# Optimization experiments

Hardware: AMD Instinct MI355X
Metric: run time of the kernel (lower is better)

Reference implementation:

```python
import math
import jax, jax.numpy as jnp
import numpy as np

B, T, D, H, KVH = 2, 2048, 2048, 16, 4
DK = D // H  # 128


def setup_inputs() -> dict:
    key = jax.random.key(0)
    ks = jax.random.split(key, 7)
    q = jax.random.normal(ks[0], (B, T, D), dtype=jnp.float32)
    k = jax.random.normal(ks[1], (B, T, D), dtype=jnp.float32)
    v = jax.random.normal(ks[2], (B, T, D), dtype=jnp.float32)
    # torch Linear weights: (out_features, in_features)
    Wq = jax.random.normal(ks[3], (D, D), dtype=jnp.float32) * 0.02
    Wk = jax.random.normal(ks[4], (KVH * DK, D), dtype=jnp.float32) * 0.02
    Wv = jax.random.normal(ks[5], (KVH * DK, D), dtype=jnp.float32) * 0.02
    Wo = jax.random.normal(ks[6], (D, D), dtype=jnp.float32) * 0.02
    # qk_norm gain, init = log(max_seq_len)
    g = jnp.full((1, H, 1, 1), math.log(2048.0), dtype=jnp.float32)
    return {"q": q, "k": k, "v": v, "Wq": Wq, "Wk": Wk, "Wv": Wv, "Wo": Wo, "g": g}


def _l2norm(x, eps=1e-12):
    # matches torch F.normalize(dim=-1): x / max(||x||, eps)
    n = jnp.sqrt(jnp.sum(x * x, axis=-1, keepdims=True))
    return x / jnp.maximum(n, eps)


def reference(q, k, v, Wq, Wk, Wv, Wo, g):
    b, tq, d = q.shape
    tk = k.shape[1]
    h = g.shape[1]
    dk = d // h
    kvh = Wk.shape[0] // dk

    Q = jnp.einsum('btd,ed->bte', q, Wq).reshape(b, tq, h, dk).transpose(0, 2, 1, 3)     # (B,H,Tq,dk)
    K = jnp.einsum('btd,ed->bte', k, Wk).reshape(b, tk, kvh, dk).transpose(0, 2, 1, 3)   # (B,KVH,Tk,dk)
    V = jnp.einsum('btd,ed->bte', v, Wv).reshape(b, tk, kvh, dk).transpose(0, 2, 1, 3)

    # QK-norm + learned per-head gain
    Q = g * _l2norm(Q)
    K = _l2norm(K)

    # GQA: repeat-interleave kv heads to match query heads (torch enable_gqa)
    rep = h // kvh
    Kr = jnp.repeat(K, rep, axis=1)
    Vr = jnp.repeat(V, rep, axis=1)

    scale = 1.0 / math.sqrt(dk)
    scores = jnp.einsum('bhqd,bhkd->bhqk', Q, Kr) * scale  # (B,H,Tq,Tk)
    causal = jnp.tril(jnp.ones((tq, tk), dtype=bool))
    scores = jnp.where(causal, scores, jnp.finfo(scores.dtype).min)
    A = jax.nn.softmax(scores, axis=-1)
    Y = jnp.einsum('bhqk,bhkd->bhqd', A, Vr)               # (B,H,Tq,dk)
    Y = Y.transpose(0, 2, 1, 3).reshape(b, tq, d)
    return jnp.einsum('btd,ed->bte', Y, Wo)
```

## Files before the change

### kernel.cpp

```cpp
#include <hip/hip_runtime.h>
#include <hip/hip_bf16.h>
#include <stdint.h>

#define B_ 2
#define T_ 2048
#define D_ 2048
#define H_ 16
#define KVH_ 4
#define DK_ 128

typedef __bf16 bf16x8 __attribute__((ext_vector_type(8)));
typedef float f32x4 __attribute__((ext_vector_type(4)));
typedef unsigned short u16x8 __attribute__((ext_vector_type(8)));

typedef __attribute__((address_space(1))) void* gas1_t;
typedef __attribute__((address_space(3))) void* gas3_t;

__device__ __forceinline__ uint16_t f2bf(float f) {
  uint32_t u = __builtin_bit_cast(uint32_t, f);
  u += 0x7FFFu + ((u >> 16) & 1u);
  return (uint16_t)(u >> 16);
}

__device__ __forceinline__ void async16(const void* g, void* l) {
  __builtin_amdgcn_global_load_lds((gas1_t)(uintptr_t)g, (gas3_t)l, 16, 0, 0);
}

__global__ __launch_bounds__(256) void k_cvt_all(const float* __restrict__ q,
                                                 const float* __restrict__ k,
                                                 const float* __restrict__ v,
                                                 const float* __restrict__ wq,
                                                 const float* __restrict__ wk,
                                                 const float* __restrict__ wv,
                                                 const float* __restrict__ wo,
                                                 uint16_t* __restrict__ qb,
                                                 uint16_t* __restrict__ kb,
                                                 uint16_t* __restrict__ vb,
                                                 uint16_t* __restrict__ wqb,
                                                 uint16_t* __restrict__ wkb,
                                                 uint16_t* __restrict__ wvb,
                                                 uint16_t* __restrict__ wob) {
  int gb = blockIdx.x;
  const float* s; uint16_t* d; int base;
  if (gb < 4096)        { s = q;  d = qb;  base = 0; }
  else if (gb < 8192)   { s = k;  d = kb;  base = 4096; }
  else if (gb < 12288)  { s = v;  d = vb;  base = 8192; }
  else if (gb < 14336)  { s = wq; d = wqb; base = 12288; }
  else if (gb < 14848)  { s = wk; d = wkb; base = 14336; }
  else if (gb < 15360)  { s = wv; d = wvb; base = 14848; }
  else                  { s = wo; d = wob; base = 15360; }
  int i = (gb - base) * 256 + threadIdx.x;
  const float4* s4 = (const float4*)s;
  float4 a = s4[(size_t)i * 2], b = s4[(size_t)i * 2 + 1];
  union { uint16_t u[8]; uint4 v; } o;
  o.u[0] = f2bf(a.x); o.u[1] = f2bf(a.y); o.u[2] = f2bf(a.z); o.u[3] = f2bf(a.w);
  o.u[4] = f2bf(b.x); o.u[5] = f2bf(b.y); o.u[6] = f2bf(b.z); o.u[7] = f2bf(b.w);
  ((uint4*)d)[i] = o.v;
}


__global__ __launch_bounds__(256) void k_gemm_bt(const uint16_t* __restrict__ A,
                                                 const uint16_t* __restrict__ Bm,
                                                 float* __restrict__ C,
                                                 int M, int N, int K) {
  __shared__ uint16_t As[2 * 128 * 64];
  __shared__ uint16_t Bs[2 * 128 * 64];
  const int tid = threadIdx.x;
  const int nt = N >> 7;
  const int m0 = (blockIdx.x / nt) << 7;
  const int n0 = (blockIdx.x % nt) << 7;
  const int w = tid >> 6, lane = tid & 63;
  const int wr = (w >> 1) << 6, wc = (w & 1) << 6;
  const int lr = lane & 15;
  const int g16 = ((lane >> 4) << 4);
  const int csw = ((lane & 1) << 6) | (((lane >> 1) & 1) << 5);
  f32x4 acc[4][4] = {};
  const int soff = tid * 16;
  const int scol = ((tid & 7) ^ (((tid >> 3) & 1) << 2) ^ (((tid >> 4) & 1) << 1)) << 3;
  const int srow = tid >> 3;
  const int nk = K >> 6;

  auto stage = [&](int t, int buf) {
    char* Ab = (char*)As + (buf << 14);
    char* Bb = (char*)Bs + (buf << 14);
#pragma unroll
    for (int i = 0; i < 4; ++i) {
      int row = i * 32 + srow;
      async16(A + (size_t)(m0 + row) * K + t * 64 + scol, Ab + i * 4096 + soff);
      async16(Bm + (size_t)(n0 + row) * K + t * 64 + scol, Bb + i * 4096 + soff);
    }
  };

  stage(0, 0);
  asm volatile("s_waitcnt vmcnt(0)" ::: "memory");
  __builtin_amdgcn_s_barrier();
  for (int t = 0; t < nk; ++t) {
    const int cur = t & 1;
    if (t + 1 < nk) stage(t + 1, cur ^ 1);
    const char* Ab = (const char*)As + (cur << 14);
    const char* Bb = (const char*)Bs + (cur << 14);
#pragma unroll
    for (int kk2 = 0; kk2 < 128; kk2 += 64) {
      bf16x8 af[4], bfr[4];
      const int cb = (kk2 + g16) ^ csw;
#pragma unroll
      for (int m = 0; m < 4; ++m)
        af[m] = *(const bf16x8*)(Ab + (wr + m * 16 + lr) * 128 + cb);
#pragma unroll
      for (int n = 0; n < 4; ++n)
        bfr[n] = *(const bf16x8*)(Bb + (wc + n * 16 + lr) * 128 + cb);
#pragma unroll
      for (int m = 0; m < 4; ++m)
#pragma unroll
        for (int n = 0; n < 4; ++n)
          acc[m][n] = __builtin_amdgcn_mfma_f32_16x16x32_bf16(af[m], bfr[n], acc[m][n], 0, 0, 0);
    }
    asm volatile("s_waitcnt vmcnt(0)" ::: "memory");
    __builtin_amdgcn_s_barrier();
  }
  const int r0 = (lane >> 4) << 2;
  const int c = lane & 15;
#pragma unroll
  for (int m = 0; m < 4; ++m)
#pragma unroll
    for (int n = 0; n < 4; ++n)
#pragma unroll
      for (int r = 0; r < 4; ++r)
        C[(size_t)(m0 + wr + m * 16 + r0 + r) * N + n0 + wc + n * 16 + c] = acc[m][n][r];
}

__global__ __launch_bounds__(256) void k_proj(const uint16_t* __restrict__ qb,
                                              const uint16_t* __restrict__ kb,
                                              const uint16_t* __restrict__ vb,
                                              const uint16_t* __restrict__ Wqb,
                                              const uint16_t* __restrict__ Wkb,
                                              const uint16_t* __restrict__ Wvb,
                                              uint16_t* __restrict__ Qn,
                                              uint16_t* __restrict__ Kn,
                                              uint16_t* __restrict__ Vt,
                                              const float* __restrict__ g) {
  __shared__ char smem[65536];
  __shared__ float ssred[2][128];
  const int bid = blockIdx.x;
  int mode, lb;
  if (bid < 128)      { mode = 2; lb = bid; }
  else if (bid < 256) { mode = 1; lb = bid - 128; }
  else                { mode = 0; lb = bid - 256; }
  const uint16_t* A;
  const uint16_t* Bw;
  int nt;
  if (mode == 0)      { A = qb; Bw = Wqb; nt = 16; }
  else if (mode == 1) { A = kb; Bw = Wkb; nt = 4; }
  else                { A = vb; Bw = Wvb; nt = 4; }
  const int m0 = (lb / nt) << 7;
  const int n0 = (lb % nt) << 7;
  const int tid = threadIdx.x;
  const int w = tid >> 6, lane = tid & 63;
  const int wr = (w >> 1) << 6, wc = (w & 1) << 6;
  const int lr = lane & 15;
  const int g16 = ((lane >> 4) << 4);
  const int csw = ((lane & 1) << 6) | (((lane >> 1) & 1) << 5);
  f32x4 acc[4][4] = {};
  const int soff = tid * 16;
  const int scol = ((tid & 7) ^ (((tid >> 3) & 1) << 2) ^ (((tid >> 4) & 1) << 1)) << 3;
  const int srow = tid >> 3;

  auto stage = [&](int t, int buf) {
    char* Ab = smem + (buf << 14);
    char* Bb = smem + 32768 + (buf << 14);
#pragma unroll
    for (int i = 0; i < 4; ++i) {
      int row = i * 32 + srow;
      async16(A + (size_t)(m0 + row) * 2048 + t * 64 + scol, Ab + i * 4096 + soff);
      async16(Bw + (size_t)(n0 + row) * 2048 + t * 64 + scol, Bb + i * 4096 + soff);
    }
  };

  stage(0, 0);
  asm volatile("s_waitcnt vmcnt(0)" ::: "memory");
  __builtin_amdgcn_s_barrier();
  for (int t = 0; t < 32; ++t) {
    const int cur = t & 1;
    if (t < 31) stage(t + 1, cur ^ 1);
    const char* Ab = (const char*)smem + (cur << 14);
    const char* Bb = (const char*)smem + 32768 + (cur << 14);
#pragma unroll
    for (int kk2 = 0; kk2 < 128; kk2 += 64) {
      bf16x8 af[4], bfr[4];
      const int cb = (kk2 + g16) ^ csw;
#pragma unroll
      for (int m = 0; m < 4; ++m)
        af[m] = *(const bf16x8*)(Ab + (wr + m * 16 + lr) * 128 + cb);
#pragma unroll
      for (int n = 0; n < 4; ++n)
        bfr[n] = *(const bf16x8*)(Bb + (wc + n * 16 + lr) * 128 + cb);
#pragma unroll
      for (int m = 0; m < 4; ++m)
#pragma unroll
        for (int n = 0; n < 4; ++n)
          acc[m][n] = __builtin_amdgcn_mfma_f32_16x16x32_bf16(af[m], bfr[n], acc[m][n], 0, 0, 0);
    }
    asm volatile("s_waitcnt vmcnt(0)" ::: "memory");
    __builtin_amdgcn_s_barrier();
  }

  const int g4 = lane >> 4;
  const int r04 = g4 << 2;
  const int b = m0 >> 11;
  const int t0 = m0 & (T_ - 1);
  const int h = n0 >> 7;

  if (mode <= 1) {
    float ss[4][4];
#pragma unroll
    for (int m = 0; m < 4; ++m)
#pragma unroll
      for (int r = 0; r < 4; ++r) {
        float s = 0.f;
#pragma unroll
        for (int n = 0; n < 4; ++n) s += acc[m][n][r] * acc[m][n][r];
        ss[m][r] = s;
      }
#pragma unroll
    for (int mask = 1; mask < 16; mask <<= 1)
#pragma unroll
      for (int m = 0; m < 4; ++m)
#pragma unroll
        for (int r = 0; r < 4; ++r) ss[m][r] += __shfl_xor(ss[m][r], mask);
#pragma unroll
    for (int m = 0; m < 4; ++m)
#pragma unroll
      for (int r = 0; r < 4; ++r)
        if (lr == (m << 2 | r)) ssred[w & 1][wr + m * 16 + g4 * 4 + r] = ss[m][r];
    __syncthreads();
    uint16_t* outp = (mode == 0) ? Qn : Kn;
    const int NHv = (mode == 0) ? H_ : KVH_;
    const float gmul = (mode == 0) ? g[h] * 0.08838834764831845f : 1.0f;
#pragma unroll
    for (int m = 0; m < 4; ++m)
#pragma unroll
      for (int r = 0; r < 4; ++r) {
        int row = wr + m * 16 + g4 * 4 + r;
        float tot = ssred[0][row] + ssred[1][row];
        float scl = gmul / fmaxf(sqrtf(tot), 1e-12f);
        size_t base = ((size_t)(b * NHv + h) * T_ + (t0 + row)) * 128;
#pragma unroll
        for (int n = 0; n < 4; ++n)
          outp[base + wc + n * 16 + lr] = f2bf(acc[m][n][r] * scl);
      }
  } else {
    uint16_t* tr = (uint16_t*)smem;
#pragma unroll
    for (int m = 0; m < 4; ++m)
#pragma unroll
      for (int n = 0; n < 4; ++n)
#pragma unroll
        for (int r = 0; r < 4; ++r)
          tr[(wc + n * 16 + lr) * 132 + (wr + m * 16 + r04 + r)] = f2bf(acc[m][n][r]);
    __syncthreads();
    const int qd = tid & 3;
#pragma unroll
    for (int dd = 0; dd < 2; ++dd) {
      int d = (tid >> 2) + dd * 64;
      uint16_t* dst = Vt + ((size_t)(b * KVH_ + h) * 128 + d) * T_ + t0 + qd * 32;
      const uint16_t* srcl = &tr[d * 132 + qd * 32];
#pragma unroll
      for (int j = 0; j < 8; ++j)
        *(ushort4*)(dst + j * 4) = *(const ushort4*)(srcl + j * 4);
    }
  }
}

__global__ __launch_bounds__(256) void k_attn(const uint16_t* __restrict__ Qn,
                                              const uint16_t* __restrict__ Kn,
                                              const uint16_t* __restrict__ Vt,
                                              uint16_t* __restrict__ Y) {
  __shared__ uint16_t Ks[2 * 64 * 128];
  __shared__ uint16_t Vs[2 * 128 * 64];
  __shared__ uint16_t Ps[4 * 16 * 32];
  const int npair = T_ / 128;
  const int pair_id = blockIdx.x % npair;
  const int bh = blockIdx.x / npair;
  const int h = bh % H_;
  const int b = bh / H_;
  const int kvh = h >> 2;
  const int qtA = pair_id;
  const int qtB = (T_ / 64) - 1 - pair_id;
  const uint16_t* Qh = Qn + ((size_t)(b * H_ + h) * T_) * 128;
  const uint16_t* Kh = Kn + ((size_t)(b * KVH_ + kvh) * T_) * 128;
  const uint16_t* Vh = Vt + ((size_t)(b * KVH_ + kvh) * 128) * T_;
  const int tid = threadIdx.x;
  const int w = tid >> 6, lane = tid & 63;
  const int lr = lane & 15;
  const int lk2 = (lane >> 4) << 4;
  const int r0 = (lane >> 4) << 2;
  const int qwA = qtA * 64 + w * 16;
  const int qwB = qtB * 64 + w * 16;
  char* Psw = (char*)Ps + w * 1024;

  bf16x8 qfA[4], qfB[4];
#pragma unroll
  for (int dblk = 0; dblk < 4; ++dblk) {
    qfA[dblk] = *(const bf16x8*)&Qh[(size_t)(qwA + lr) * 128 + dblk * 32 + (lk2 >> 1)];
    qfB[dblk] = *(const bf16x8*)&Qh[(size_t)(qwB + lr) * 128 + dblk * 32 + (lk2 >> 1)];
  }
  union { uint16_t u[8]; bf16x8 v; } ou;
#pragma unroll
  for (int j = 0; j < 8; ++j) ou.u[j] = 0x3F80;
  const bf16x8 ones = ou.v;
  f32x4 oA[8] = {}, oB[8] = {};
  f32x4 sumA = {}, sumB = {};

  auto stageKV = [&](int tile, int buf) {
    const int kv0 = tile * 64;
    char* Kb = (char*)Ks + (buf << 14);
    char* Vb = (char*)Vs + (buf << 14);
#pragma unroll
    for (int i = 0; i < 4; ++i) {
      int off = i * 4096 + tid * 16;
      int krow = off >> 8;
      int kchunk = (off >> 4) & 15;
      int kcol = (kchunk ^ (krow & 7)) << 3;
      async16(Kh + (size_t)(kv0 + krow) * 128 + kcol, Kb + off);
      int vrow = off >> 7;
      int vchunk = (off >> 4) & 7;
      int vcol = (vchunk ^ (vrow & 7)) << 3;
      async16(Vh + (size_t)vrow * T_ + kv0 + vcol, Vb + off);
    }
  };

  auto tilecompute = [&](const bf16x8* qf, f32x4* o, f32x4* sum, int qw, int kv0, int cur) {
    const char* Kb = (const char*)Ks + (cur << 14);
    const char* Vb = (const char*)Vs + (cur << 14);
#pragma unroll
    for (int prr = 0; prr < 2; ++prr) {
#pragma unroll
      for (int kbi = 0; kbi < 2; ++kbi) {
        int kb = prr * 2 + kbi;
        f32x4 s = {};
#pragma unroll
        for (int dblk = 0; dblk < 4; ++dblk) {
          bf16x8 kf = *(const bf16x8*)(Kb +
              ((kb * 16 + lr) << 8) + ((dblk * 64 + lk2) ^ ((lr & 7) << 4)));
          s = __builtin_amdgcn_mfma_f32_16x16x32_bf16(qf[dblk], kf, s, 0, 0, 0);
        }
        int kval = kv0 + kb * 16 + lr;
#pragma unroll
        for (int r = 0; r < 4; ++r) {
          float pv = (kval <= qw + r0 + r) ? __expf(s[r]) : 0.0f;
          *(uint16_t*)(Psw + (r0 + r) * 64 + (((kbi * 16 + lr) * 2) ^ (r << 4))) = f2bf(pv);
        }
      }
      asm volatile("s_waitcnt lgkmcnt(0)" ::: "memory");
      bf16x8 pa = *(const bf16x8*)(Psw + lr * 64 + (lk2 ^ ((lr & 3) << 4)));
#pragma unroll
      for (int dblk = 0; dblk < 8; ++dblk) {
        bf16x8 vf = *(const bf16x8*)(Vb +
            ((dblk * 16 + lr) << 7) + ((prr * 64 + lk2) ^ ((lr & 7) << 4)));
        o[dblk] = __builtin_amdgcn_mfma_f32_16x16x32_bf16(pa, vf, o[dblk], 0, 0, 0);
      }
      *sum = __builtin_amdgcn_mfma_f32_16x16x32_bf16(pa, ones, *sum, 0, 0, 0);
    }
  };

  stageKV(0, 0);
  asm volatile("s_waitcnt vmcnt(0)" ::: "memory");
  __builtin_amdgcn_s_barrier();
  for (int tile = 0; tile <= qtB; ++tile) {
    const int cur = tile & 1;
    if (tile < qtB) stageKV(tile + 1, cur ^ 1);
    const int kv0 = tile * 64;
    tilecompute(qfB, oB, &sumB, qwB, kv0, cur);
    if (tile <= qtA) tilecompute(qfA, oA, &sumA, qwA, kv0, cur);
    asm volatile("s_waitcnt vmcnt(0)" ::: "memory");
    __builtin_amdgcn_s_barrier();
  }

  auto writeout = [&](const f32x4* o, const f32x4& sum, int qw) {
#pragma unroll
    for (int r = 0; r < 4; ++r) {
      float inv = 1.0f / sum[r];
      size_t base = ((size_t)b * T_ + (qw + r0 + r)) * D_ + h * 128 + lr;
#pragma unroll
      for (int dblk = 0; dblk < 8; ++dblk)
        Y[base + dblk * 16] = f2bf(o[dblk][r] * inv);
    }
  };
  writeout(oA, sumA, qwA);
  writeout(oB, sumB, qwB);
}

extern "C" void kernel_launch(void* const* d_in, const int* in_sizes, int n_in,
                              void* d_out, int out_size, void* d_ws, size_t ws_size,
                              hipStream_t stream) {
  (void)in_sizes; (void)n_in; (void)out_size; (void)ws_size;
  const float* q  = (const float*)d_in[0];
  const float* k  = (const float*)d_in[1];
  const float* v  = (const float*)d_in[2];
  const float* Wq = (const float*)d_in[3];
  const float* Wk = (const float*)d_in[4];
  const float* Wv = (const float*)d_in[5];
  const float* Wo = (const float*)d_in[6];
  const float* g  = (const float*)d_in[7];
  float* out = (float*)d_out;
  char* ws = (char*)d_ws;
  const size_t MB = 1ull << 20;
  uint16_t* qb  = (uint16_t*)(ws);
  uint16_t* kb  = (uint16_t*)(ws + 16 * MB);
  uint16_t* vb  = (uint16_t*)(ws + 32 * MB);
  uint16_t* Wqb = (uint16_t*)(ws + 48 * MB);
  uint16_t* Wkb = (uint16_t*)(ws + 56 * MB);
  uint16_t* Wvb = (uint16_t*)(ws + 58 * MB);
  uint16_t* Kn  = (uint16_t*)(ws + 60 * MB);
  uint16_t* Vtb = (uint16_t*)(ws + 64 * MB);
  uint16_t* Wob = (uint16_t*)(ws + 68 * MB);
  uint16_t* Qn  = (uint16_t*)d_out;
  uint16_t* Y   = qb;

  k_cvt_all<<<17408, 256, 0, stream>>>(q, k, v, Wq, Wk, Wv, Wo,
                                       qb, kb, vb, Wqb, Wkb, Wvb, Wob);
  k_proj<<<768, 256, 0, stream>>>(qb, kb, vb, Wqb, Wkb, Wvb, Qn, Kn, Vtb, g);
  k_attn<<<B_ * H_ * (T_ / 128), 256, 0, stream>>>(Qn, Kn, Vtb, Y);
  k_gemm_bt<<<(B_ * T_ / 128) * (D_ / 128), 256, 0, stream>>>(Y, Wob, out, B_ * T_, D_, D_);
}
```

Measured before the change: 222.4 us.

## Use 256x128 GEMM tiles with single-buffered LDS in projection and output GEMMs

Doubles the M dimension of each block tile in the projection and output GEMMs so each B tile is reused across two A sub-tiles. Double buffering is replaced by a single LDS buffer with a load-then-sync schedule, and occupancy hints are added. This aims to cut global/LDS traffic per MFMA, but halves the block count and removes load/compute overlap. The fused norm and V-transpose epilogues are adapted to the taller tile.

```diff
diff --git a/kernel.cpp b/kernel.cpp
--- a/kernel.cpp
+++ b/kernel.cpp
@@ -59,100 +59,93 @@
 }
 
 
-__global__ __launch_bounds__(256) void k_gemm_bt(const uint16_t* __restrict__ A,
-                                                 const uint16_t* __restrict__ Bm,
-                                                 float* __restrict__ C,
-                                                 int M, int N, int K) {
-  __shared__ uint16_t As[2 * 128 * 64];
-  __shared__ uint16_t Bs[2 * 128 * 64];
+__global__ __launch_bounds__(256, 2) void k_gemm_bt(const uint16_t* __restrict__ A,
+                                                    const uint16_t* __restrict__ Bm,
+                                                    float* __restrict__ C,
+                                                    int M, int N, int K) {
+  __shared__ char smem[49152];
   const int tid = threadIdx.x;
   const int nt = N >> 7;
-  const int m0 = (blockIdx.x / nt) << 7;
+  const int m0 = (blockIdx.x / nt) << 8;
   const int n0 = (blockIdx.x % nt) << 7;
   const int w = tid >> 6, lane = tid & 63;
   const int wr = (w >> 1) << 6, wc = (w & 1) << 6;
   const int lr = lane & 15;
   const int g16 = ((lane >> 4) << 4);
   const int csw = ((lane & 1) << 6) | (((lane >> 1) & 1) << 5);
-  f32x4 acc[4][4] = {};
+  f32x4 acc[8][4] = {};
   const int soff = tid * 16;
   const int scol = ((tid & 7) ^ (((tid >> 3) & 1) << 2) ^ (((tid >> 4) & 1) << 1)) << 3;
   const int srow = tid >> 3;
   const int nk = K >> 6;
 
-  auto stage = [&](int t, int buf) {
-    char* Ab = (char*)As + (buf << 14);
-    char* Bb = (char*)Bs + (buf << 14);
+  for (int t = 0; t < nk; ++t) {
 #pragma unroll
     for (int i = 0; i < 4; ++i) {
       int row = i * 32 + srow;
-      async16(A + (size_t)(m0 + row) * K + t * 64 + scol, Ab + i * 4096 + soff);
-      async16(Bm + (size_t)(n0 + row) * K + t * 64 + scol, Bb + i * 4096 + soff);
-    }
-  };
-
-  stage(0, 0);
-  asm volatile("s_waitcnt vmcnt(0)" ::: "memory");
-  __builtin_amdgcn_s_barrier();
-  for (int t = 0; t < nk; ++t) {
-    const int cur = t & 1;
-    if (t + 1 < nk) stage(t + 1, cur ^ 1);
-    const char* Ab = (const char*)As + (cur << 14);
-    const char* Bb = (const char*)Bs + (cur << 14);
+      async16(A + (size_t)(m0 + row) * K + t * 64 + scol, smem + i * 4096 + soff);
+      async16(A + (size_t)(m0 + 128 + row) * K + t * 64 + scol, smem + 16384 + i * 4096 + soff);
+      async16(Bm + (size_t)(n0 + row) * K + t * 64 + scol, smem + 32768 + i * 4096 + soff);
+    }
+    __syncthreads();
 #pragma unroll
     for (int kk2 = 0; kk2 < 128; kk2 += 64) {
-      bf16x8 af[4], bfr[4];
+      bf16x8 aA[4], aB[4], bfr[4];
       const int cb = (kk2 + g16) ^ csw;
 #pragma unroll
+      for (int m = 0; m < 4; ++m) {
+        aA[m] = *(const bf16x8*)(smem + (wr + m * 16 + lr) * 128 + cb);
+        aB[m] = *(const bf16x8*)(smem + 16384 + (wr + m * 16 + lr) * 128 + cb);
+      }
+#pragma unroll
+      for (int n = 0; n < 4; ++n)
+        bfr[n] = *(const bf16x8*)(smem + 32768 + (wc + n * 16 + lr) * 128 + cb);
+#pragma unroll
       for (int m = 0; m < 4; ++m)
-        af[m] = *(const bf16x8*)(Ab + (wr + m * 16 + lr) * 128 + cb);
-#pragma unroll
-      for (int n = 0; n < 4; ++n)
-        bfr[n] = *(const bf16x8*)(Bb + (wc + n * 16 + lr) * 128 + cb);
-#pragma unroll
-      for (int m = 0; m < 4; ++m)
-#pragma unroll
-        for (int n = 0; n < 4; ++n)
-          acc[m][n] = __builtin_amdgcn_mfma_f32_16x16x32_bf16(af[m], bfr[n], acc[m][n], 0, 0, 0);
-    }
-    asm volatile("s_waitcnt vmcnt(0)" ::: "memory");
-    __builtin_amdgcn_s_barrier();
+#pragma unroll
+        for (int n = 0; n < 4; ++n) {
+          acc[m][n] = __builtin_amdgcn_mfma_f32_16x16x32_bf16(aA[m], bfr[n], acc[m][n], 0, 0, 0);
+          acc[m + 4][n] = __builtin_amdgcn_mfma_f32_16x16x32_bf16(aB[m], bfr[n], acc[m + 4][n], 0, 0, 0);
+        }
+    }
+    __syncthreads();
   }
   const int r0 = (lane >> 4) << 2;
   const int c = lane & 15;
 #pragma unroll
-  for (int m = 0; m < 4; ++m)
+  for (int m = 0; m < 8; ++m)
 #pragma unroll
     for (int n = 0; n < 4; ++n)
 #pragma unroll
       for (int r = 0; r < 4; ++r)
-        C[(size_t)(m0 + wr + m * 16 + r0 + r) * N + n0 + wc + n * 16 + c] = acc[m][n][r];
-}
-
-__global__ __launch_bounds__(256) void k_proj(const uint16_t* __restrict__ qb,
-                                              const uint16_t* __restrict__ kb,
-                                              const uint16_t* __restrict__ vb,
-                                              const uint16_t* __restrict__ Wqb,
-                                              const uint16_t* __restrict__ Wkb,
-                                              const uint16_t* __restrict__ Wvb,
-                                              uint16_t* __restrict__ Qn,
-                                              uint16_t* __restrict__ Kn,
-                                              uint16_t* __restrict__ Vt,
-                                              const float* __restrict__ g) {
-  __shared__ char smem[65536];
-  __shared__ float ssred[2][128];
+        C[(size_t)(m0 + (m >> 2) * 128 + wr + (m & 3) * 16 + r0 + r) * N +
+          n0 + wc + n * 16 + c] = acc[m][n][r];
+}
+
+__global__ __launch_bounds__(256, 2) void k_proj(const uint16_t* __restrict__ qb,
+                                                 const uint16_t* __restrict__ kb,
+                                                 const uint16_t* __restrict__ vb,
+                                                 const uint16_t* __restrict__ Wqb,
+                                                 const uint16_t* __restrict__ Wkb,
+                                                 const uint16_t* __restrict__ Wvb,
+                                                 uint16_t* __restrict__ Qn,
+                                                 uint16_t* __restrict__ Kn,
+                                                 uint16_t* __restrict__ Vt,
+                                                 const float* __restrict__ g) {
+  __shared__ char smem[49152];
+  __shared__ float ssred[2][256];
   const int bid = blockIdx.x;
   int mode, lb;
-  if (bid < 128)      { mode = 2; lb = bid; }
-  else if (bid < 256) { mode = 1; lb = bid - 128; }
-  else                { mode = 0; lb = bid - 256; }
+  if (bid < 64)       { mode = 2; lb = bid; }
+  else if (bid < 128) { mode = 1; lb = bid - 64; }
+  else                { mode = 0; lb = bid - 128; }
   const uint16_t* A;
   const uint16_t* Bw;
   int nt;
   if (mode == 0)      { A = qb; Bw = Wqb; nt = 16; }
   else if (mode == 1) { A = kb; Bw = Wkb; nt = 4; }
   else                { A = vb; Bw = Wvb; nt = 4; }
-  const int m0 = (lb / nt) << 7;
+  const int m0 = (lb / nt) << 8;
   const int n0 = (lb % nt) << 7;
   const int tid = threadIdx.x;
   const int w = tid >> 6, lane = tid & 63;
@@ -160,48 +153,41 @@
   const int lr = lane & 15;
   const int g16 = ((lane >> 4) << 4);
   const int csw = ((lane & 1) << 6) | (((lane >> 1) & 1) << 5);
-  f32x4 acc[4][4] = {};
+  f32x4 acc[8][4] = {};
   const int soff = tid * 16;
   const int scol = ((tid & 7) ^ (((tid >> 3) & 1) << 2) ^ (((tid >> 4) & 1) << 1)) << 3;
   const int srow = tid >> 3;
 
-  auto stage = [&](int t, int buf) {
-    char* Ab = smem + (buf << 14);
-    char* Bb = smem + 32768 + (buf << 14);
+  for (int t = 0; t < 32; ++t) {
 #pragma unroll
     for (int i = 0; i < 4; ++i) {
       int row = i * 32 + srow;
-      async16(A + (size_t)(m0 + row) * 2048 + t * 64 + scol, Ab + i * 4096 + soff);
-      async16(Bw + (size_t)(n0 + row) * 2048 + t * 64 + scol, Bb + i * 4096 + soff);
-    }
-  };
-
-  stage(0, 0);
-  asm volatile("s_waitcnt vmcnt(0)" ::: "memory");
-  __builtin_amdgcn_s_barrier();
-  for (int t = 0; t < 32; ++t) {
-    const int cur = t & 1;
-    if (t < 31) stage(t + 1, cur ^ 1);
-    const char* Ab = (const char*)smem + (cur << 14);
-    const char* Bb = (const char*)smem + 32768 + (cur << 14);
+      async16(A + (size_t)(m0 + row) * 2048 + t * 64 + scol, smem + i * 4096 + soff);
+      async16(A + (size_t)(m0 + 128 + row) * 2048 + t * 64 + scol, smem + 16384 + i * 4096 + soff);
+      async16(Bw + (size_t)(n0 + row) * 2048 + t * 64 + scol, smem + 32768 + i * 4096 + soff);
+    }
+    __syncthreads();
 #pragma unroll
     for (int kk2 = 0; kk2 < 128; kk2 += 64) {
-      bf16x8 af[4], bfr[4];
+      bf16x8 aA[4], aB[4], bfr[4];
       const int cb = (kk2 + g16) ^ csw;
 #pragma unroll
+      for (int m = 0; m < 4; ++m) {
+        aA[m] = *(const bf16x8*)(smem + (wr + m * 16 + lr) * 128 + cb);
+        aB[m] = *(const bf16x8*)(smem + 16384 + (wr + m * 16 + lr) * 128 + cb);
+      }
+#pragma unroll
+      for (int n = 0; n < 4; ++n)
+        bfr[n] = *(const bf16x8*)(smem + 32768 + (wc + n * 16 + lr) * 128 + cb);
+#pragma unroll
       for (int m = 0; m < 4; ++m)
-        af[m] = *(const bf16x8*)(Ab + (wr + m * 16 + lr) * 128 + cb);
-#pragma unroll
-      for (int n = 0; n < 4; ++n)
-        bfr[n] = *(const bf16x8*)(Bb + (wc + n * 16 + lr) * 128 + cb);
-#pragma unroll
-      for (int m = 0; m < 4; ++m)
-#pragma unroll
-        for (int n = 0; n < 4; ++n)
-          acc[m][n] = __builtin_amdgcn_mfma_f32_16x16x32_bf16(af[m], bfr[n], acc[m][n], 0, 0, 0);
-    }
-    asm volatile("s_waitcnt vmcnt(0)" ::: "memory");
-    __builtin_amdgcn_s_barrier();
+#pragma unroll
+        for (int n = 0; n < 4; ++n) {
+          acc[m][n] = __builtin_amdgcn_mfma_f32_16x16x32_bf16(aA[m], bfr[n], acc[m][n], 0, 0, 0);
+          acc[m + 4][n] = __builtin_amdgcn_mfma_f32_16x16x32_bf16(aB[m], bfr[n], acc[m + 4][n], 0, 0, 0);
+        }
+    }
+    __syncthreads();
   }
 
   const int g4 = lane >> 4;
@@ -211,9 +197,9 @@
   const int h = n0 >> 7;
 
   if (mode <= 1) {
-    float ss[4][4];
-#pragma unroll
-    for (int m = 0; m < 4; ++m)
+    float ss[8][4];
+#pragma unroll
+    for (int m = 0; m < 8; ++m)
 #pragma unroll
       for (int r = 0; r < 4; ++r) {
         float s = 0.f;
@@ -224,23 +210,24 @@
 #pragma unroll
     for (int mask = 1; mask < 16; mask <<= 1)
 #pragma unroll
-      for (int m = 0; m < 4; ++m)
+      for (int m = 0; m < 8; ++m)
 #pragma unroll
         for (int r = 0; r < 4; ++r) ss[m][r] += __shfl_xor(ss[m][r], mask);
 #pragma unroll
-    for (int m = 0; m < 4; ++m)
+    for (int m = 0; m < 8; ++m)
 #pragma unroll
       for (int r = 0; r < 4; ++r)
-        if (lr == (m << 2 | r)) ssred[w & 1][wr + m * 16 + g4 * 4 + r] = ss[m][r];
+        if (lr == (((m & 3) << 2) | r))
+          ssred[w & 1][(m >> 2) * 128 + wr + (m & 3) * 16 + g4 * 4 + r] = ss[m][r];
     __syncthreads();
     uint16_t* outp = (mode == 0) ? Qn : Kn;
     const int NHv = (mode == 0) ? H_ : KVH_;
     const float gmul = (mode == 0) ? g[h] * 0.08838834764831845f : 1.0f;
 #pragma unroll
-    for (int m = 0; m < 4; ++m)
+    for (int m = 0; m < 8; ++m)
 #pragma unroll
       for (int r = 0; r < 4; ++r) {
-        int row = wr + m * 16 + g4 * 4 + r;
+        int row = (m >> 2) * 128 + wr + (m & 3) * 16 + g4 * 4 + r;
         float tot = ssred[0][row] + ssred[1][row];
         float scl = gmul / fmaxf(sqrtf(tot), 1e-12f);
         size_t base = ((size_t)(b * NHv + h) * T_ + (t0 + row)) * 128;
@@ -251,22 +238,26 @@
   } else {
     uint16_t* tr = (uint16_t*)smem;
 #pragma unroll
-    for (int m = 0; m < 4; ++m)
-#pragma unroll
-      for (int n = 0; n < 4; ++n)
-#pragma unroll
-        for (int r = 0; r < 4; ++r)
-          tr[(wc + n * 16 + lr) * 132 + (wr + m * 16 + r04 + r)] = f2bf(acc[m][n][r]);
-    __syncthreads();
-    const int qd = tid & 3;
-#pragma unroll
-    for (int dd = 0; dd < 2; ++dd) {
-      int d = (tid >> 2) + dd * 64;
-      uint16_t* dst = Vt + ((size_t)(b * KVH_ + h) * 128 + d) * T_ + t0 + qd * 32;
-      const uint16_t* srcl = &tr[d * 132 + qd * 32];
-#pragma unroll
-      for (int j = 0; j < 8; ++j)
-        *(ushort4*)(dst + j * 4) = *(const ushort4*)(srcl + j * 4);
+    for (int p = 0; p < 2; ++p) {
+      __syncthreads();
+#pragma unroll
+      for (int mm = 0; mm < 4; ++mm)
+#pragma unroll
+        for (int n = 0; n < 4; ++n)
+#pragma unroll
+          for (int r = 0; r < 4; ++r)
+            tr[(wc + n * 16 + lr) * 132 + (wr + mm * 16 + r04 + r)] = f2bf(acc[p * 4 + mm][n][r]);
+      __syncthreads();
+      const int qd = tid & 3;
+#pragma unroll
+      for (int dd = 0; dd < 2; ++dd) {
+        int d = (tid >> 2) + dd * 64;
+        uint16_t* dst = Vt + ((size_t)(b * KVH_ + h) * 128 + d) * T_ + t0 + p * 128 + qd * 32;
+        const uint16_t* srcl = &tr[d * 132 + qd * 32];
+#pragma unroll
+        for (int j = 0; j < 8; ++j)
+          *(ushort4*)(dst + j * 4) = *(const ushort4*)(srcl + j * 4);
+      }
     }
   }
 }
@@ -419,7 +410,7 @@
 
   k_cvt_all<<<17408, 256, 0, stream>>>(q, k, v, Wq, Wk, Wv, Wo,
                                        qb, kb, vb, Wqb, Wkb, Wvb, Wob);
-  k_proj<<<768, 256, 0, stream>>>(qb, kb, vb, Wqb, Wkb, Wvb, Qn, Kn, Vtb, g);
+  k_proj<<<384, 256, 0, stream>>>(qb, kb, vb, Wqb, Wkb, Wvb, Qn, Kn, Vtb, g);
   k_attn<<<B_ * H_ * (T_ / 128), 256, 0, stream>>>(Qn, Kn, Vtb, Y);
-  k_gemm_bt<<<(B_ * T_ / 128) * (D_ / 128), 256, 0, stream>>>(Y, Wob, out, B_ * T_, D_, D_);
-}
+  k_gemm_bt<<<(B_ * T_ / 256) * (D_ / 128), 256, 0, stream>>>(Y, Wob, out, B_ * T_, D_, D_);
+}
```

New measurement: 219.7 us. About the same (-1.2%).

## Swizzle GEMM block order for L2 reuse and switch to full XOR LDS swizzle

Applied to the files above, without the earlier changes.

Remaps block indices in the output GEMM and the projection kernel into 8x8 groups of M-panels and N-tiles, so concurrently running blocks share A and B tiles in L2. Replaces the partial LDS column swizzle with a full 3-bit XOR swizzle on row, applied to both the staging writes and the fragment reads, to reduce LDS bank conflicts. Reorders the projection launch so the large Q blocks are scheduled first, ahead of V and K. The block mapping hardcodes the grid shapes, which ties the GEMM kernel to specific M and N.

```diff
diff --git a/kernel.cpp b/kernel.cpp
--- a/kernel.cpp
+++ b/kernel.cpp
@@ -66,17 +66,17 @@
   __shared__ uint16_t As[2 * 128 * 64];
   __shared__ uint16_t Bs[2 * 128 * 64];
   const int tid = threadIdx.x;
-  const int nt = N >> 7;
-  const int m0 = (blockIdx.x / nt) << 7;
-  const int n0 = (blockIdx.x % nt) << 7;
+  const int x = blockIdx.x & 7, j = blockIdx.x >> 3;
+  const int m0 = (((x >> 1) << 3) + (j & 7)) << 7;
+  const int n0 = (((x & 1) << 3) + (j >> 3)) << 7;
   const int w = tid >> 6, lane = tid & 63;
   const int wr = (w >> 1) << 6, wc = (w & 1) << 6;
   const int lr = lane & 15;
   const int g16 = ((lane >> 4) << 4);
-  const int csw = ((lane & 1) << 6) | (((lane >> 1) & 1) << 5);
+  const int lsw = (lr & 7) << 4;
   f32x4 acc[4][4] = {};
   const int soff = tid * 16;
-  const int scol = ((tid & 7) ^ (((tid >> 3) & 1) << 2) ^ (((tid >> 4) & 1) << 1)) << 3;
+  const int scol = ((tid & 7) ^ ((tid >> 3) & 7)) << 3;
   const int srow = tid >> 3;
   const int nk = K >> 6;
 
@@ -102,7 +102,7 @@
 #pragma unroll
     for (int kk2 = 0; kk2 < 128; kk2 += 64) {
       bf16x8 af[4], bfr[4];
-      const int cb = (kk2 + g16) ^ csw;
+      const int cb = (kk2 + g16) ^ lsw;
 #pragma unroll
       for (int m = 0; m < 4; ++m)
         af[m] = *(const bf16x8*)(Ab + (wr + m * 16 + lr) * 128 + cb);
@@ -139,35 +139,43 @@
                                               uint16_t* __restrict__ Kn,
                                               uint16_t* __restrict__ Vt,
                                               const float* __restrict__ g) {
-  __shared__ char smem[65536];
+  __shared__ uint16_t As[2 * 128 * 64];
+  __shared__ uint16_t Bs[2 * 128 * 64];
   __shared__ float ssred[2][128];
   const int bid = blockIdx.x;
   int mode, lb;
-  if (bid < 128)      { mode = 2; lb = bid; }
-  else if (bid < 256) { mode = 1; lb = bid - 128; }
-  else                { mode = 0; lb = bid - 256; }
+  if (bid < 512)      { mode = 0; lb = bid; }
+  else if (bid < 640) { mode = 2; lb = bid - 512; }
+  else                { mode = 1; lb = bid - 640; }
   const uint16_t* A;
   const uint16_t* Bw;
-  int nt;
-  if (mode == 0)      { A = qb; Bw = Wqb; nt = 16; }
-  else if (mode == 1) { A = kb; Bw = Wkb; nt = 4; }
-  else                { A = vb; Bw = Wvb; nt = 4; }
-  const int m0 = (lb / nt) << 7;
-  const int n0 = (lb % nt) << 7;
+  if (mode == 0)      { A = qb; Bw = Wqb; }
+  else if (mode == 1) { A = kb; Bw = Wkb; }
+  else                { A = vb; Bw = Wvb; }
+  int mpanel, ntile;
+  {
+    int x = lb & 7, jj = lb >> 3;
+    if (mode == 0) { mpanel = ((x >> 1) << 3) + (jj & 7); ntile = ((x & 1) << 3) + (jj >> 3); }
+    else           { mpanel = ((x >> 1) << 3) + (jj & 7); ntile = ((x & 1) << 1) + (jj >> 3); }
+  }
+  const int m0 = mpanel << 7;
+  const int n0 = ntile << 7;
   const int tid = threadIdx.x;
   const int w = tid >> 6, lane = tid & 63;
   const int wr = (w >> 1) << 6, wc = (w & 1) << 6;
   const int lr = lane & 15;
   const int g16 = ((lane >> 4) << 4);
-  const int csw = ((lane & 1) << 6) | (((lane >> 1) & 1) << 5);
+  const int lsw = (lr & 7) << 4;
   f32x4 acc[4][4] = {};
   const int soff = tid * 16;
-  const int scol = ((tid & 7) ^ (((tid >> 3) & 1) << 2) ^ (((tid >> 4) & 1) << 1)) << 3;
+  const int scol = ((tid & 7) ^ ((tid >> 3) & 7)) << 3;
   const int srow = tid >> 3;
+  const int g4 = lane >> 4;
+  const int r04 = g4 << 2;
 
   auto stage = [&](int t, int buf) {
-    char* Ab = smem + (buf << 14);
-    char* Bb = smem + 32768 + (buf << 14);
+    char* Ab = (char*)As + (buf << 14);
+    char* Bb = (char*)Bs + (buf << 14);
 #pragma unroll
     for (int i = 0; i < 4; ++i) {
       int row = i * 32 + srow;
@@ -181,13 +189,13 @@
   __builtin_amdgcn_s_barrier();
   for (int t = 0; t < 32; ++t) {
     const int cur = t & 1;
-    if (t < 31) stage(t + 1, cur ^ 1);
-    const char* Ab = (const char*)smem + (cur << 14);
-    const char* Bb = (const char*)smem + 32768 + (cur << 14);
+    if (t + 1 < 32) stage(t + 1, cur ^ 1);
+    const char* Ab = (const char*)As + (cur << 14);
+    const char* Bb = (const char*)Bs + (cur << 14);
 #pragma unroll
     for (int kk2 = 0; kk2 < 128; kk2 += 64) {
       bf16x8 af[4], bfr[4];
-      const int cb = (kk2 + g16) ^ csw;
+      const int cb = (kk2 + g16) ^ lsw;
 #pragma unroll
       for (int m = 0; m < 4; ++m)
         af[m] = *(const bf16x8*)(Ab + (wr + m * 16 + lr) * 128 + cb);
@@ -204,8 +212,6 @@
     __builtin_amdgcn_s_barrier();
   }
 
-  const int g4 = lane >> 4;
-  const int r04 = g4 << 2;
   const int b = m0 >> 11;
   const int t0 = m0 & (T_ - 1);
   const int h = n0 >> 7;
@@ -249,7 +255,7 @@
           outp[base + wc + n * 16 + lr] = f2bf(acc[m][n][r] * scl);
       }
   } else {
-    uint16_t* tr = (uint16_t*)smem;
+    uint16_t* tr = (uint16_t*)As;
 #pragma unroll
     for (int m = 0; m < 4; ++m)
 #pragma unroll
```

Result: faster. 217.1 us (-2.4%).
